# Performance work log

Measured on AMD Instinct MI355X. Metric: run time of the kernel, lower is better.

## Reference

```python
import jax, jax.numpy as jnp
import numpy as np

B, S, D = 8, 4096, 1024
CAPACITY = 0.75
K = max(1, int(S * CAPACITY))  # 3072


def setup_inputs() -> dict:
    key = jax.random.key(0)
    k1, k2, k3 = jax.random.split(key, 3)
    x = jax.random.normal(k1, (B, S, D), dtype=jnp.float32)
    processed = jax.random.normal(k2, (B, K, D), dtype=jnp.float32)
    w_router = jax.random.normal(k3, (D,), dtype=jnp.float32) * 0.02
    return {"x": x, "processed": processed, "w_router": w_router}


def reference(x, processed, w_router):
    # --- MoDRouter.forward ---
    bsz, seq_len, dim = x.shape
    k = processed.shape[1]
    # scores: (B, S) = Linear(dim -> 1, no bias)
    scores = jnp.einsum('bsd,d->bs', x, w_router)
    # top-k per batch row, sorted descending (matches torch.topk sorted=True)
    topk_scores, indices = jax.lax.top_k(scores, k)  # (B, K)
    # gather routed tokens: (B, K, D)
    routed_x = jnp.take_along_axis(x, indices[:, :, None], axis=1)
    # --- MoDRouter.scatter_back (processed = block output for routed tokens) ---
    weights = jax.nn.softmax(topk_scores, axis=1)[:, :, None]  # (B, K, 1)
    # original values at routed positions == routed_x (same gather)
    blended = processed * weights + (1.0 - weights) * routed_x  # (B, K, D)
    batch_idx = jnp.arange(bsz)[:, None]  # (B, 1)
    output = x.at[batch_idx, indices].set(blended)  # unrouted positions keep x
    return output
```

## Files before the change

### kernel.cpp

```cpp
#include <hip/hip_runtime.h>
#include <math.h>

#define BB 8
#define SS 4096
#define DD 1024
#define KK 3072
#define NCHUNK 8
#define CHUNK 512
#define NELEM (BB * SS)

typedef unsigned long long u64;
typedef unsigned int u32;

__global__ __launch_bounds__(256) void mod_scores(const float* __restrict__ x,
                                                  const float* __restrict__ w,
                                                  float* __restrict__ scores,
                                                  u64* __restrict__ keys) {
    int wave = (int)((blockIdx.x * blockDim.x + threadIdx.x) >> 6);
    int lane = threadIdx.x & 63;
    if (wave >= NELEM) return;
    const float4* xr = (const float4*)(x + (size_t)wave * DD);
    const float4* wr = (const float4*)w;
    float acc = 0.f;
#pragma unroll
    for (int i = 0; i < 4; ++i) {
        float4 a = xr[lane + 64 * i];
        float4 b = wr[lane + 64 * i];
        acc += a.x * b.x + a.y * b.y + a.z * b.z + a.w * b.w;
    }
#pragma unroll
    for (int off = 32; off > 0; off >>= 1)
        acc += __shfl_down(acc, off, 64);
    if (lane == 0) {
        scores[wave] = acc;
        u32 u = __float_as_uint(acc);
        u32 m = (u & 0x80000000u) ? ~u : (u | 0x80000000u);
        keys[wave] = ((u64)(~m) << 32) | (u32)(wave & (SS - 1));
    }
}

__global__ __launch_bounds__(256) void mod_rank_partial(const u64* __restrict__ keys,
                                                        int* __restrict__ pcnt) {
    __shared__ u64 lk[CHUNK];
    const int ob = blockIdx.x / NCHUNK;
    const int c  = blockIdx.x - ob * NCHUNK;
    const int tid = threadIdx.x;
    const int gid = ob * 256 + tid;
    const int b = gid >> 12;

    const u64* __restrict__ cand = keys + ((size_t)b << 12) + c * CHUNK;
    lk[tid]       = cand[tid];
    lk[tid + 256] = cand[tid + 256];
    __syncthreads();

    const u64 my = keys[gid];
    int cnt = 0;
#pragma unroll 8
    for (int k = 0; k < CHUNK; ++k)
        cnt += (lk[k] < my) ? 1 : 0;
    pcnt[c * NELEM + gid] = cnt;
}

__global__ __launch_bounds__(256) void mod_finalize(const int* __restrict__ pcnt,
                                                    const float* __restrict__ scores,
                                                    int* __restrict__ rank_of,
                                                    float* __restrict__ partial) {
    const int gid = blockIdx.x * 256 + threadIdx.x;
    int r = 0;
#pragma unroll
    for (int c = 0; c < NCHUNK; ++c) r += pcnt[c * NELEM + gid];
    rank_of[gid] = r;

    float e = (r < KK) ? expf(scores[gid]) : 0.f;
    __shared__ float red[256];
    red[threadIdx.x] = e;
    __syncthreads();
    for (int off = 128; off > 0; off >>= 1) {
        if (threadIdx.x < off) red[threadIdx.x] += red[threadIdx.x + off];
        __syncthreads();
    }
    if (threadIdx.x == 0) partial[blockIdx.x] = red[0];
}

__global__ __launch_bounds__(256) void mod_blend(const float* __restrict__ x,
                                                 const float* __restrict__ proc,
                                                 const int* __restrict__ rank_of,
                                                 const float* __restrict__ scores,
                                                 const float* __restrict__ partial,
                                                 float* __restrict__ out) {
    const int row = blockIdx.x;
    const int b = row >> 12;
    const int t = threadIdx.x;
    const float4* xr = (const float4*)(x + (size_t)row * DD);
    float4* orow = (float4*)(out + (size_t)row * DD);
    const int j = rank_of[row];
    float4 a = xr[t];
    if (j < KK) {
        float denom = 0.f;
#pragma unroll
        for (int i = 0; i < 16; ++i) denom += partial[b * 16 + i];
        float w = expf(scores[row]) / denom;
        const float4* pr = (const float4*)(proc + ((size_t)b * KK + j) * DD);
        float4 p = pr[t];
        float4 o;
        o.x = p.x * w + (1.f - w) * a.x;
        o.y = p.y * w + (1.f - w) * a.y;
        o.z = p.z * w + (1.f - w) * a.z;
        o.w = p.w * w + (1.f - w) * a.w;
        orow[t] = o;
    } else {
        orow[t] = a;
    }
}

extern "C" void kernel_launch(void* const* d_in, const int* in_sizes, int n_in,
                              void* d_out, int out_size, void* d_ws, size_t ws_size,
                              hipStream_t stream) {
    const float* x    = (const float*)d_in[0];
    const float* proc = (const float*)d_in[1];
    const float* w    = (const float*)d_in[2];
    float* out = (float*)d_out;

    u64*   keys    = (u64*)d_ws;
    float* scores  = (float*)((char*)d_ws + NELEM * 8);
    int*   rank_of = (int*)((char*)d_ws + NELEM * 12);
    int*   pcnt    = (int*)((char*)d_ws + NELEM * 16);
    float* partial = (float*)((char*)d_ws + NELEM * 16 + NELEM * 4 * NCHUNK);

    mod_scores      <<<NELEM / 4, 256, 0, stream>>>(x, w, scores, keys);
    mod_rank_partial<<<(NELEM / 256) * NCHUNK, 256, 0, stream>>>(keys, pcnt);
    mod_finalize    <<<NELEM / 256, 256, 0, stream>>>(pcnt, scores, rank_of, partial);
    mod_blend       <<<NELEM, 256, 0, stream>>>(x, proc, rank_of, scores, partial, out);
}
```

Before: 94.10 us.

## Count ranks with wave ballots over lane-distributed candidates instead of per-thread LDS scans

The rank-counting kernel no longer has each thread scan all 512 shared-memory candidates. Each lane now loads one candidate per 64-wide group, and for every query key broadcast via readlane the wave does a ballot/popcount compare. This reduces LDS reads per thread from 512 to 8. The trade is many more ballot and popcount instructions, uniform 64-bit compares across lanes, and a select chain to hand each count back to its lane. The shared-memory fill also becomes a single 16-byte vector load per thread.

```diff
diff --git a/kernel.cpp b/kernel.cpp
--- a/kernel.cpp
+++ b/kernel.cpp
@@ -41,24 +41,45 @@
 
 __global__ __launch_bounds__(256) void mod_rank_partial(const u64* __restrict__ keys,
                                                         int* __restrict__ pcnt) {
-    __shared__ u64 lk[CHUNK];
+    __shared__ __align__(16) u64 lk[CHUNK];
     const int ob = blockIdx.x / NCHUNK;
     const int c  = blockIdx.x - ob * NCHUNK;
     const int tid = threadIdx.x;
     const int gid = ob * 256 + tid;
     const int b = gid >> 12;
+    const int lane = tid & 63;
 
     const u64* __restrict__ cand = keys + ((size_t)b << 12) + c * CHUNK;
-    lk[tid]       = cand[tid];
-    lk[tid + 256] = cand[tid + 256];
+    *(ulonglong2*)&lk[tid * 2] = *(const ulonglong2*)&cand[tid * 2];
     __syncthreads();
 
     const u64 my = keys[gid];
-    int cnt = 0;
-#pragma unroll 8
-    for (int k = 0; k < CHUNK; ++k)
-        cnt += (lk[k] < my) ? 1 : 0;
-    pcnt[c * NELEM + gid] = cnt;
+    const u32 my_hi = (u32)(my >> 32);
+    const u32 my_lo = (u32)my;
+
+    int v_cnt = 0;
+#pragma unroll
+    for (int g = 0; g < 8; ++g) {
+        u64 mj[8];
+#pragma unroll
+        for (int j = 0; j < 8; ++j) {
+            u32 h = (u32)__builtin_amdgcn_readlane((int)my_hi, g * 8 + j);
+            u32 l = (u32)__builtin_amdgcn_readlane((int)my_lo, g * 8 + j);
+            mj[j] = ((u64)h << 32) | l;
+        }
+        int cnt[8] = {0, 0, 0, 0, 0, 0, 0, 0};
+#pragma unroll
+        for (int cg = 0; cg < CHUNK / 64; ++cg) {
+            u64 cv = lk[cg * 64 + lane];
+#pragma unroll
+            for (int j = 0; j < 8; ++j)
+                cnt[j] += (int)__popcll(__ballot(cv < mj[j]));
+        }
+#pragma unroll
+        for (int j = 0; j < 8; ++j)
+            v_cnt = (lane == g * 8 + j) ? cnt[j] : v_cnt;
+    }
+    pcnt[c * NELEM + gid] = v_cnt;
 }
 
 __global__ __launch_bounds__(256) void mod_finalize(const int* __restrict__ pcnt,
```

Measured after the change: 93.34 us. Within noise of the previous version (-0.8%).
